# Kernel optimization log

Measured on AMD Instinct MI355X. Metric: run time of the kernel, lower is better.

## Reference

```python
import jax, jax.numpy as jnp
import numpy as np

B, T, NT, H, L, F, NH, R = 2, 1024, 30, 1024, 8, 2816, 16, 16
HD = H // NH
LORA_SCALE = 32.0 / 16.0  # lora_alpha / r
CLAMP = 10.0
EPS = 1e-6


def _rms(x, w):
    return x * jax.lax.rsqrt(jnp.mean(x * x, axis=-1, keepdims=True) + EPS) * w


def _rope(x):
    # x: [B,T,NH,HD] -- LLaMA rotary embedding
    half = HD // 2
    inv_freq = 1.0 / (10000.0 ** (jnp.arange(0, half, dtype=jnp.float32) / half))
    ang = jnp.arange(x.shape[1], dtype=jnp.float32)[:, None] * inv_freq  # [T,half]
    cos = jnp.concatenate([jnp.cos(ang), jnp.cos(ang)], -1)[None, :, None, :]
    sin = jnp.concatenate([jnp.sin(ang), jnp.sin(ang)], -1)[None, :, None, :]
    x1, x2 = x[..., :half], x[..., half:]
    return x * cos + jnp.concatenate([-x2, x1], -1) * sin


def _lora(x, W, A, Bm):
    # W: [in,out], A: [r,in], Bm: [out,r]  (dequantized base + LoRA update)
    return x @ W + ((x @ A.T) @ Bm.T) * LORA_SCALE


def setup_inputs():
    key = jax.random.key(0)
    ks = jax.random.split(key, 16)
    n = lambda k, s, sc=0.02: jax.random.normal(k, s, jnp.float32) * sc
    return {
        'x': jax.random.normal(ks[0], (B, T, NT), jnp.float32),
        'temperature': jnp.float32(1.0),
        'state_W': n(ks[1], (NT, H), 0.1),
        'state_b': jnp.zeros((H,), jnp.float32),
        'ln1': jnp.ones((L, H), jnp.float32),
        'ln2': jnp.ones((L, H), jnp.float32),
        'Wqkv': n(ks[2], (L, 3, H, H)),
        'Aqkv': n(ks[3], (L, 3, R, H)),
        'Bqkv': n(ks[4], (L, 3, H, R)),
        'Wo': n(ks[5], (L, H, H)),
        'Ao': n(ks[6], (L, R, H)),
        'Bo': n(ks[7], (L, H, R)),
        'Wgu': n(ks[8], (L, 2, H, F)),
        'Agu': n(ks[9], (L, 2, R, H)),
        'Bgu': n(ks[10], (L, 2, F, R)),
        'Wd': n(ks[11], (L, F, H)),
        'Ad': n(ks[12], (L, R, F)),
        'Bd': n(ks[13], (L, H, R)),
        'ln_f': jnp.ones((H,), jnp.float32),
        'head_W': n(ks[14], (H, NT + 1), 0.01),
        'head_b': jnp.zeros((NT + 1,), jnp.float32),
    }


def reference(x, temperature, state_W, state_b, ln1, ln2, Wqkv, Aqkv, Bqkv,
              Wo, Ao, Bo, Wgu, Agu, Bgu, Wd, Ad, Bd, ln_f, head_W, head_b):
    causal = jnp.tril(jnp.ones((T, T), bool))

    def layer(h, p):
        l1, l2, wqkv, aqkv, bqkv, wo, ao, bo, wgu, agu, bgu, wd, ad, bd = p
        hn = _rms(h, l1)
        qkv = jnp.einsum('bth,khd->kbtd', hn, wqkv)
        qkv = qkv + jnp.einsum('kbtr,kdr->kbtd',
                               jnp.einsum('bth,krh->kbtr', hn, aqkv), bqkv) * LORA_SCALE
        q = _rope(qkv[0].reshape(B, T, NH, HD))
        k = _rope(qkv[1].reshape(B, T, NH, HD))
        v = qkv[2].reshape(B, T, NH, HD)
        scores = jnp.einsum('bqhd,bkhd->bhqk', q, k) / np.sqrt(HD).astype(np.float32)
        scores = jnp.where(causal, scores, jnp.float32(-1e9))
        probs = jax.nn.softmax(scores, axis=-1)
        att = jnp.einsum('bhqk,bkhd->bqhd', probs, v).reshape(B, T, H)
        h = h + _lora(att, wo, ao, bo)
        hn2 = _rms(h, l2)
        gu = jnp.einsum('bth,khf->kbtf', hn2, wgu)
        gu = gu + jnp.einsum('kbtr,kfr->kbtf',
                             jnp.einsum('bth,krh->kbtr', hn2, agu), bgu) * LORA_SCALE
        act = jax.nn.silu(gu[0]) * gu[1]
        h = h + _lora(act, wd, ad, bd)
        return h, None

    h = x @ state_W + state_b  # state encoder -> inputs_embeds
    h, _ = jax.lax.scan(layer, h, (ln1, ln2, Wqkv, Aqkv, Bqkv, Wo, Ao, Bo,
                                   Wgu, Agu, Bgu, Wd, Ad, Bd))
    latent = _rms(h, ln_f)  # last hidden state
    logits = latent @ head_W + head_b
    logits_clamped = jnp.clip(logits, -CLAMP, CLAMP)
    portfolio_weights = jax.nn.softmax(logits_clamped / temperature, axis=-1)
    return portfolio_weights, logits_clamped
```

## Files before the change

### kernel.cpp

```cpp
#include <hip/hip_runtime.h>
#include <hip/hip_bf16.h>
#include <cstdint>

#define B_    2
#define T_    1024
#define NT_   30
#define H_    1024
#define L_    8
#define F_    2816
#define NH_   16
#define R_    16
#define HD_   64
#define M_    2048
#define NTP1_ 31

typedef unsigned short u16;
typedef short  s16x8 __attribute__((ext_vector_type(8)));
typedef unsigned short u16x4 __attribute__((ext_vector_type(4)));
typedef unsigned short u16x8 __attribute__((ext_vector_type(8)));
typedef float  f32x4 __attribute__((ext_vector_type(4)));

__device__ __forceinline__ u16 f2bf(float f){
  __hip_bfloat16 h = __float2bfloat16(f);
  return __builtin_bit_cast(unsigned short, h);
}
__device__ __forceinline__ float bf2f(u16 u){
  uint32_t v = (uint32_t)u << 16;
  return __builtin_bit_cast(float, v);
}

__device__ __forceinline__ void async16(const void* g, void* l){
  __builtin_amdgcn_global_load_lds((const __attribute__((address_space(1))) void*)g,
                                   (__attribute__((address_space(3))) void*)l, 16, 0, 0);
}

__global__ __launch_bounds__(256, 3) void fold_kernel(
    const float* __restrict__ W, const float* __restrict__ A,
    const float* __restrict__ Bm, u16* __restrict__ Wt,
    int K, int N, long strW, long strA, long strB, long strWt)
{
  const int mat = blockIdx.z;
  W  += (long)mat * strW;  A  += (long)mat * strA;
  Bm += (long)mat * strB;  Wt += (long)mat * strWt;
  const int k0 = blockIdx.x * 64, n0 = blockIdx.y * 64;
  __shared__ float Wt_s[64][65];
  __shared__ float As[16][64];
  __shared__ float Bs[64][20];
  const int tid = threadIdx.x;
  {
    const int kr = tid >> 4;
    const int n4 = (tid & 15) * 4;
    #pragma unroll
    for (int p = 0; p < 4; p++){
      int krow = p * 16 + kr;
      float4 w = *(const float4*)(W + (long)(k0 + krow) * N + n0 + n4);
      Wt_s[n4+0][krow] = w.x; Wt_s[n4+1][krow] = w.y;
      Wt_s[n4+2][krow] = w.z; Wt_s[n4+3][krow] = w.w;
    }
    const int r = tid >> 4, kc = (tid & 15) * 4;
    *(float4*)&As[r][kc] = *(const float4*)(A + (long)r * K + k0 + kc);
    const int nb = tid >> 2, r4 = (tid & 3) * 4;
    float4 b = *(const float4*)(Bm + (long)(n0 + nb) * 16 + r4);
    Bs[nb][r4+0]=b.x; Bs[nb][r4+1]=b.y; Bs[nb][r4+2]=b.z; Bs[nb][r4+3]=b.w;
  }
  __syncthreads();
  const int ko = (tid & 7) * 8;
  const int na = tid >> 3;
  float bq0[16], bq1[16];
  #pragma unroll
  for (int c = 0; c < 4; c++){
    *(float4*)&bq0[c*4] = *(const float4*)&Bs[na][c*4];
    *(float4*)&bq1[c*4] = *(const float4*)&Bs[na+32][c*4];
  }
  float l0[8] = {}, l1[8] = {};
  #pragma unroll
  for (int r = 0; r < 16; r++){
    float a[8];
    *(float4*)&a[0] = *(const float4*)&As[r][ko];
    *(float4*)&a[4] = *(const float4*)&As[r][ko+4];
    #pragma unroll
    for (int j = 0; j < 8; j++){
      l0[j] += a[j] * bq0[r];
      l1[j] += a[j] * bq1[r];
    }
  }
  u16x8 o0, o1;
  #pragma unroll
  for (int j = 0; j < 8; j++){
    o0[j] = f2bf(Wt_s[na][ko+j]    + 2.0f * l0[j]);
    o1[j] = f2bf(Wt_s[na+32][ko+j] + 2.0f * l1[j]);
  }
  *(u16x8*)(Wt + (long)(n0+na)*K    + k0 + ko) = o0;
  *(u16x8*)(Wt + (long)(n0+na+32)*K + k0 + ko) = o1;
}

__global__ __launch_bounds__(256) void embed_kernel(
    const float* __restrict__ x, const float* __restrict__ sw,
    const float* __restrict__ sb, float* __restrict__ h)
{
  const int m = blockIdx.x;
  const float* xr = x + (long)m * NT_;
  for (int jj = threadIdx.x; jj < H_; jj += 256){
    float acc = sb[jj];
    #pragma unroll
    for (int i = 0; i < NT_; i++) acc += xr[i] * sw[i * H_ + jj];
    h[(long)m * H_ + jj] = acc;
  }
}

__global__ __launch_bounds__(256) void rms_kernel(
    float* __restrict__ hsrc, const float* __restrict__ p0, const float* __restrict__ p1,
    const float* __restrict__ w, u16* __restrict__ outp, int fuse)
{
  const int m = blockIdx.x, t = threadIdx.x;
  float4 v = ((const float4*)(hsrc + (long)m * H_))[t];
  if (fuse){
    const float4 a = ((const float4*)(p0 + (long)m * H_))[t];
    const float4 b = ((const float4*)(p1 + (long)m * H_))[t];
    v.x += a.x + b.x; v.y += a.y + b.y; v.z += a.z + b.z; v.w += a.w + b.w;
    ((float4*)(hsrc + (long)m * H_))[t] = v;
  }
  float ss = v.x*v.x + v.y*v.y + v.z*v.z + v.w*v.w;
  #pragma unroll
  for (int off = 32; off >= 1; off >>= 1) ss += __shfl_xor(ss, off);
  __shared__ float red[4];
  if ((t & 63) == 0) red[t >> 6] = ss;
  __syncthreads();
  const float scale = rsqrtf((red[0]+red[1]+red[2]+red[3]) * (1.0f/H_) + 1e-6f);
  const float4 wv = ((const float4*)w)[t];
  u16x4 o;
  o[0] = f2bf(v.x*scale*wv.x); o[1] = f2bf(v.y*scale*wv.y);
  o[2] = f2bf(v.z*scale*wv.z); o[3] = f2bf(v.w*scale*wv.w);
  *(u16x4*)(outp + (long)m * H_ + t * 4) = o;
}

template<int OUTBF>
__global__ __launch_bounds__(256, 2) void gemm_bt(
    const u16* __restrict__ Ag, const u16* __restrict__ Btg, void* __restrict__ Cptr,
    int Ndim, int Klen, int Kstride, long zsA, long zsB, long zsC)
{
  Ag  += (long)blockIdx.z * zsA;
  Btg += (long)blockIdx.z * zsB;
  const int m0 = blockIdx.x * 128, n0 = blockIdx.y * 128;
  __shared__ alignas(16) u16 As[128 * 64];
  __shared__ alignas(16) u16 Bs[128 * 64];
  const int tid = threadIdx.x;
  const int wave = tid >> 6, lane = tid & 63;
  const int wm = (wave & 1) * 64, wn = (wave >> 1) * 64;
  const int fr = lane & 15, quad = lane >> 4;

  f32x4 acc[4][4] = {};

  for (int kt = 0; kt < Klen; kt += 64){
    __syncthreads();
    #pragma unroll
    for (int c = 0; c < 4; c++){
      int lin = c * 256 + tid;
      int row = lin >> 3, p = lin & 7;
      int gc = ((p ^ (row & 7)) * 8);
      async16(Ag  + (long)(m0 + row) * Kstride + kt + gc, As + lin * 8);
      async16(Btg + (long)(n0 + row) * Kstride + kt + gc, Bs + lin * 8);
    }
    __syncthreads();
    #pragma unroll
    for (int kk = 0; kk < 2; kk++){
      s16x8 af[4], bg[4];
      #pragma unroll
      for (int i = 0; i < 4; i++){
        int rA = wm + i * 16 + fr;
        af[i] = *(const s16x8*)(As + rA * 64 + (((kk*4 + quad) ^ (rA & 7)) * 8));
        int rB = wn + i * 16 + fr;
        bg[i] = *(const s16x8*)(Bs + rB * 64 + (((kk*4 + quad) ^ (rB & 7)) * 8));
      }
      #pragma unroll
      for (int i = 0; i < 4; i++)
        #pragma unroll
        for (int j = 0; j < 4; j++)
          acc[i][j] = __builtin_amdgcn_mfma_f32_16x16x32_bf16(af[i], bg[j], acc[i][j], 0, 0, 0);
    }
  }
  #pragma unroll
  for (int i = 0; i < 4; i++){
    int row0 = m0 + wm + i * 16 + quad * 4;
    #pragma unroll
    for (int j = 0; j < 4; j++){
      int col = n0 + wn + j * 16 + fr;
      #pragma unroll
      for (int r = 0; r < 4; r++){
        long idx = (long)(row0 + r) * Ndim + col;
        if (OUTBF){
          u16* C = (u16*)Cptr + (long)blockIdx.z * zsC;
          C[idx] = f2bf(acc[i][j][r]);
        } else {
          float* C = (float*)Cptr + (long)blockIdx.z * zsC;
          C[idx] = acc[i][j][r];
        }
      }
    }
  }
}

__global__ __launch_bounds__(256, 2) void gemm_gu(
    const u16* __restrict__ Ag, const u16* __restrict__ Bgw,
    const u16* __restrict__ Buw, u16* __restrict__ actb)
{
  const int m0 = blockIdx.x * 128, n0 = blockIdx.y * 128;
  __shared__ alignas(16) u16 As[128 * 64];
  __shared__ alignas(16) u16 Bg_[128 * 64];
  __shared__ alignas(16) u16 Bu_[128 * 64];
  const int tid = threadIdx.x;
  const int wave = tid >> 6, lane = tid & 63;
  const int wm = (wave & 1) * 64, wn = (wave >> 1) * 64;
  const int fr = lane & 15, quad = lane >> 4;

  f32x4 accg[4][4] = {}, accu[4][4] = {};

  for (int kt = 0; kt < H_; kt += 64){
    __syncthreads();
    #pragma unroll
    for (int c = 0; c < 4; c++){
      int lin = c * 256 + tid;
      int row = lin >> 3, p = lin & 7;
      int gc = ((p ^ (row & 7)) * 8);
      async16(Ag  + (long)(m0 + row) * H_ + kt + gc, As  + lin * 8);
      async16(Bgw + (long)(n0 + row) * H_ + kt + gc, Bg_ + lin * 8);
      async16(Buw + (long)(n0 + row) * H_ + kt + gc, Bu_ + lin * 8);
    }
    __syncthreads();
    #pragma unroll
    for (int kk = 0; kk < 2; kk++){
      s16x8 af[4], bb[4];
      #pragma unroll
      for (int i = 0; i < 4; i++){
        int rA = wm + i * 16 + fr;
        af[i] = *(const s16x8*)(As + rA * 64 + (((kk*4 + quad) ^ (rA & 7)) * 8));
      }
      #pragma unroll
      for (int i = 0; i < 4; i++){
        int rB = wn + i * 16 + fr;
        bb[i] = *(const s16x8*)(Bg_ + rB * 64 + (((kk*4 + quad) ^ (rB & 7)) * 8));
      }
      #pragma unroll
      for (int i = 0; i < 4; i++)
        #pragma unroll
        for (int j = 0; j < 4; j++)
          accg[i][j] = __builtin_amdgcn_mfma_f32_16x16x32_bf16(af[i], bb[j], accg[i][j], 0, 0, 0);
      #pragma unroll
      for (int i = 0; i < 4; i++){
        int rB = wn + i * 16 + fr;
        bb[i] = *(const s16x8*)(Bu_ + rB * 64 + (((kk*4 + quad) ^ (rB & 7)) * 8));
      }
      #pragma unroll
      for (int i = 0; i < 4; i++)
        #pragma unroll
        for (int j = 0; j < 4; j++)
          accu[i][j] = __builtin_amdgcn_mfma_f32_16x16x32_bf16(af[i], bb[j], accu[i][j], 0, 0, 0);
    }
  }
  #pragma unroll
  for (int i = 0; i < 4; i++){
    int row0 = m0 + wm + i * 16 + quad * 4;
    #pragma unroll
    for (int j = 0; j < 4; j++){
      int col = n0 + wn + j * 16 + fr;
      #pragma unroll
      for (int r = 0; r < 4; r++){
        float g = accg[i][j][r], u = accu[i][j][r];
        float act = g / (1.0f + __expf(-g)) * u;
        actb[(long)(row0 + r) * F_ + col] = f2bf(act);
      }
    }
  }
}

__global__ __launch_bounds__(256) void rope_kernel(
    const u16* __restrict__ qkv, u16* __restrict__ qr, u16* __restrict__ kr)
{
  const int m = blockIdx.x;
  const int b = m >> 10, t = m & 1023;
  for (int w = threadIdx.x; w < 1024; w += 256){
    const int sel = w >> 9;
    const int hh  = (w >> 5) & 15;
    const int i   = w & 31;
    const u16* src = qkv + (long)sel * M_ * H_ + (long)m * H_ + hh * HD_;
    float x1 = bf2f(src[i]), x2 = bf2f(src[i + 32]);
    float freq = exp2f((float)i * (-13.287712379549449f / 32.0f));
    float ang = (float)t * freq;
    float sn, cs; __sincosf(ang, &sn, &cs);
    u16* dst = (sel ? kr : qr) + ((long)((b * NH_ + hh) * T_ + t)) * HD_;
    dst[i]      = f2bf(x1 * cs - x2 * sn);
    dst[i + 32] = f2bf(x2 * cs + x1 * sn);
  }
}

__global__ __launch_bounds__(256) void vtrans_kernel(
    const u16* __restrict__ qkv, u16* __restrict__ vt)
{
  const int bh = blockIdx.x, b = bh >> 4, hh = bh & 15;
  const int d = threadIdx.x & 63, tc = threadIdx.x >> 6;
  const int t0 = blockIdx.y * 32 + tc * 8;
  const u16* src = qkv + (long)2 * M_ * H_ + (long)b * T_ * H_ + hh * HD_ + d;
  u16x8 o;
  #pragma unroll
  for (int j = 0; j < 8; j++) o[j] = src[(long)(t0 + j) * H_];
  *(u16x8*)(vt + ((long)bh * HD_ + d) * T_ + t0) = o;
}

__global__ __launch_bounds__(256, 2) void attn_kernel(
    const u16* __restrict__ qr, const u16* __restrict__ kr,
    const u16* __restrict__ vt, u16* __restrict__ att)
{
  const int qt = blockIdx.x;
  const int bh = blockIdx.y;
  const int b = bh >> 4, hh = bh & 15;
  __shared__ alignas(16) u16 Qs[64 * 64];
  __shared__ alignas(16) u16 Ks[128 * 64];
  __shared__ alignas(16) u16 Vs[64 * 128];
  __shared__ alignas(16) u16 Ps[64 * 136];
  const int tid = threadIdx.x;
  const int wave = tid >> 6, lane = tid & 63, fr = lane & 15, quad = lane >> 4;
  const int wrow = wave * 16;

  const u16* qg = qr + ((long)bh * T_ + qt * 64) * HD_;
  #pragma unroll
  for (int c = 0; c < 2; c++){
    int lin = c * 256 + tid, row = lin >> 3, p = lin & 7;
    async16(qg + row * HD_ + ((p ^ (row & 7)) * 8), Qs + lin * 8);
  }
  f32x4 o_acc[4] = {};
  float m_r[4] = {-1e30f, -1e30f, -1e30f, -1e30f};
  float l_r[4] = {};
  const u16* kgb = kr + (long)bh * T_ * HD_;
  const u16* vgb = vt + (long)bh * HD_ * T_;
  const int kmax = (qt * 64 + 63) >> 7;

  for (int kt = 0; kt <= kmax; kt++){
    __syncthreads();
    const u16* kg = kgb + (long)kt * 128 * HD_;
    #pragma unroll
    for (int c = 0; c < 4; c++){
      int lin = c * 256 + tid, row = lin >> 3, p = lin & 7;
      async16(kg + row * HD_ + ((p ^ (row & 7)) * 8), Ks + lin * 8);
    }
    #pragma unroll
    for (int c = 0; c < 4; c++){
      int lin = c * 256 + tid, row = lin >> 4, p = lin & 15;
      async16(vgb + (long)row * T_ + kt * 128 + ((p ^ (row & 15)) * 8), Vs + lin * 8);
    }
    __syncthreads();

    f32x4 s[8] = {};
    s16x8 aq[2];
    {
      int rA = wrow + fr;
      #pragma unroll
      for (int kk = 0; kk < 2; kk++)
        aq[kk] = *(const s16x8*)(Qs + rA * 64 + (((kk*4 + quad) ^ (rA & 7)) * 8));
    }
    #pragma unroll
    for (int ik = 0; ik < 8; ik++){
      #pragma unroll
      for (int kk = 0; kk < 2; kk++){
        int rB = ik * 16 + fr;
        s16x8 bk = *(const s16x8*)(Ks + rB * 64 + (((kk*4 + quad) ^ (rB & 7)) * 8));
        s[ik] = __builtin_amdgcn_mfma_f32_16x16x32_bf16(aq[kk], bk, s[ik], 0, 0, 0);
      }
    }
    const bool diag = (kt == kmax);
    #pragma unroll
    for (int r = 0; r < 4; r++){
      const int qgi = qt * 64 + wrow + quad * 4 + r;
      float tmax = -1e30f;
      #pragma unroll
      for (int ik = 0; ik < 8; ik++){
        float v = s[ik][r] * 0.125f;
        if (diag && (kt * 128 + ik * 16 + fr) > qgi) v = -1e9f;
        s[ik][r] = v;
        tmax = fmaxf(tmax, v);
      }
      #pragma unroll
      for (int off = 8; off >= 1; off >>= 1) tmax = fmaxf(tmax, __shfl_xor(tmax, off));
      const float mnew = fmaxf(m_r[r], tmax);
      const float alpha = __expf(m_r[r] - mnew);
      m_r[r] = mnew;
      float ts = 0.0f;
      const int prow = wrow + quad * 4 + r;
      #pragma unroll
      for (int ik = 0; ik < 8; ik++){
        float p = __expf(s[ik][r] - mnew);
        ts += p;
        Ps[prow * 136 + ik * 16 + fr] = f2bf(p);
      }
      #pragma unroll
      for (int off = 8; off >= 1; off >>= 1) ts += __shfl_xor(ts, off);
      l_r[r] = l_r[r] * alpha + ts;
      #pragma unroll
      for (int jd = 0; jd < 4; jd++) o_acc[jd][r] *= alpha;
    }
    #pragma unroll
    for (int kk2 = 0; kk2 < 4; kk2++){
      s16x8 ap = *(const s16x8*)(Ps + (wrow + fr) * 136 + kk2 * 32 + quad * 8);
      #pragma unroll
      for (int jd = 0; jd < 4; jd++){
        int rV = jd * 16 + fr;
        s16x8 bv = *(const s16x8*)(Vs + rV * 128 + (((kk2*4 + quad) ^ (rV & 15)) * 8));
        o_acc[jd] = __builtin_amdgcn_mfma_f32_16x16x32_bf16(ap, bv, o_acc[jd], 0, 0, 0);
      }
    }
  }
  #pragma unroll
  for (int r = 0; r < 4; r++){
    const int t_loc = qt * 64 + wrow + quad * 4 + r;
    const long rowbase = ((long)b * T_ + t_loc) * H_ + hh * HD_;
    const float inv = 1.0f / l_r[r];
    #pragma unroll
    for (int jd = 0; jd < 4; jd++)
      att[rowbase + jd * 16 + fr] = f2bf(o_acc[jd][r] * inv);
  }
}

__global__ __launch_bounds__(256) void head_kernel(
    const float* __restrict__ hsrc, const float* __restrict__ p0, const float* __restrict__ p1,
    const float* __restrict__ lnf, const float* __restrict__ hw, const float* __restrict__ hb,
    const float* __restrict__ temp, float* __restrict__ outp)
{
  const int m = blockIdx.x, t = threadIdx.x;
  __shared__ float lat[H_];
  __shared__ float red[4];
  __shared__ float part[8][32];
  float4 v = ((const float4*)(hsrc + (long)m * H_))[t];
  {
    const float4 a = ((const float4*)(p0 + (long)m * H_))[t];
    const float4 b = ((const float4*)(p1 + (long)m * H_))[t];
    v.x += a.x + b.x; v.y += a.y + b.y; v.z += a.z + b.z; v.w += a.w + b.w;
  }
  float ss = v.x*v.x + v.y*v.y + v.z*v.z + v.w*v.w;
  #pragma unroll
  for (int off = 32; off >= 1; off >>= 1) ss += __shfl_xor(ss, off);
  if ((t & 63) == 0) red[t >> 6] = ss;
  __syncthreads();
  const float scale = rsqrtf((red[0]+red[1]+red[2]+red[3]) * (1.0f/H_) + 1e-6f);
  const float4 wv = ((const float4*)lnf)[t];
  lat[t*4+0] = v.x*scale*wv.x;  lat[t*4+1] = v.y*scale*wv.y;
  lat[t*4+2] = v.z*scale*wv.z;  lat[t*4+3] = v.w*scale*wv.w;
  __syncthreads();
  const int j = t & 31, seg = t >> 5;
  float p = 0.0f;
  if (j < 31){
    const float* wp = hw + j;
    for (int k = seg * 128; k < seg * 128 + 128; k++) p += lat[k] * wp[(long)k * 31];
  }
  part[seg][j] = p;
  __syncthreads();
  if (t < 32){
    float dot = 0.0f;
    #pragma unroll
    for (int s2 = 0; s2 < 8; s2++) dot += part[s2][t];
    const float logit = (t < 31) ? dot + hb[t] : -1e30f;
    const float lc = fminf(fmaxf(logit, -10.0f), 10.0f);
    const float z = (t < 31) ? lc / temp[0] : -1e30f;
    float mx = z;
    #pragma unroll
    for (int off = 16; off >= 1; off >>= 1) mx = fmaxf(mx, __shfl_xor(mx, off, 32));
    const float e = (t < 31) ? __expf(z - mx) : 0.0f;
    float sum = e;
    #pragma unroll
    for (int off = 16; off >= 1; off >>= 1) sum += __shfl_xor(sum, off, 32);
    if (t < 31){
      outp[(long)m * NTP1_ + t] = e / sum;
      outp[(long)M_ * NTP1_ + (long)m * NTP1_ + t] = lc;
    }
  }
}

extern "C" void kernel_launch(void* const* d_in, const int* in_sizes, int n_in,
                              void* d_out, int out_size, void* d_ws, size_t ws_size,
                              hipStream_t stream) {
  const float* x    = (const float*)d_in[0];
  const float* temp = (const float*)d_in[1];
  const float* sW   = (const float*)d_in[2];
  const float* sb   = (const float*)d_in[3];
  const float* ln1  = (const float*)d_in[4];
  const float* ln2  = (const float*)d_in[5];
  const float* Wqkv = (const float*)d_in[6];
  const float* Aqkv = (const float*)d_in[7];
  const float* Bqkv = (const float*)d_in[8];
  const float* Wo   = (const float*)d_in[9];
  const float* Ao   = (const float*)d_in[10];
  const float* Bo   = (const float*)d_in[11];
  const float* Wgu  = (const float*)d_in[12];
  const float* Agu  = (const float*)d_in[13];
  const float* Bgu  = (const float*)d_in[14];
  const float* Wd   = (const float*)d_in[15];
  const float* Ad   = (const float*)d_in[16];
  const float* Bd   = (const float*)d_in[17];
  const float* lnf  = (const float*)d_in[18];
  const float* hW   = (const float*)d_in[19];
  const float* hb   = (const float*)d_in[20];
  float* out = (float*)d_out;

  uint8_t* ws = (uint8_t*)d_ws;
  size_t off = 0;
  auto alloc = [&](size_t bytes) -> void* {
    void* p = ws + off;
    off += (bytes + 255) & ~(size_t)255;
    return p;
  };
  u16*   wt_qkv = (u16*)  alloc((size_t)L_ * 3 * H_ * H_ * 2);
  u16*   wt_o   = (u16*)  alloc((size_t)L_ * H_ * H_ * 2);
  u16*   wt_gu  = (u16*)  alloc((size_t)L_ * 2 * F_ * H_ * 2);
  u16*   wt_d   = (u16*)  alloc((size_t)L_ * H_ * F_ * 2);
  float* h      = (float*)alloc((size_t)M_ * H_ * 4);
  u16*   hn     = (u16*)  alloc((size_t)M_ * H_ * 2);
  u16*   qkvb   = (u16*)  alloc((size_t)3 * M_ * H_ * 2);
  float* p0     = (float*)alloc((size_t)2 * M_ * H_ * 4);
  float* p1     = p0 + (size_t)M_ * H_;
  u16*   qr     = (u16*)  alloc((size_t)M_ * H_ * 2);
  u16*   krr    = (u16*)  alloc((size_t)M_ * H_ * 2);
  u16*   vtb    = (u16*)  alloc((size_t)M_ * H_ * 2);
  u16*   attb   = (u16*)  alloc((size_t)M_ * H_ * 2);
  u16*   actb   = (u16*)  alloc((size_t)M_ * F_ * 2);

  fold_kernel<<<dim3(16, 16, L_ * 3), 256, 0, stream>>>(Wqkv, Aqkv, Bqkv, wt_qkv,
      H_, H_, (long)H_ * H_, (long)R_ * H_, (long)H_ * R_, (long)H_ * H_);
  fold_kernel<<<dim3(16, 16, L_), 256, 0, stream>>>(Wo, Ao, Bo, wt_o,
      H_, H_, (long)H_ * H_, (long)R_ * H_, (long)H_ * R_, (long)H_ * H_);
  fold_kernel<<<dim3(16, 44, L_ * 2), 256, 0, stream>>>(Wgu, Agu, Bgu, wt_gu,
      H_, F_, (long)H_ * F_, (long)R_ * H_, (long)F_ * R_, (long)F_ * H_);
  fold_kernel<<<dim3(44, 16, L_), 256, 0, stream>>>(Wd, Ad, Bd, wt_d,
      F_, H_, (long)F_ * H_, (long)R_ * F_, (long)H_ * R_, (long)H_ * F_);

  embed_kernel<<<M_, 256, 0, stream>>>(x, sW, sb, h);

  for (int l = 0; l < L_; l++){
    rms_kernel<<<M_, 256, 0, stream>>>(h, p0, p1, ln1 + (long)l * H_, hn, l > 0 ? 1 : 0);
    gemm_bt<1><<<dim3(16, 8, 3), 256, 0, stream>>>(hn, wt_qkv + (long)l * 3 * H_ * H_,
        qkvb, H_, H_, H_, 0, (long)H_ * H_, (long)M_ * H_);
    rope_kernel<<<M_, 256, 0, stream>>>(qkvb, qr, krr);
    vtrans_kernel<<<dim3(B_ * NH_, T_ / 32), 256, 0, stream>>>(qkvb, vtb);
    attn_kernel<<<dim3(T_ / 64, B_ * NH_), 256, 0, stream>>>(qr, krr, vtb, attb);
    gemm_bt<0><<<dim3(16, 8, 2), 256, 0, stream>>>(attb, wt_o + (long)l * H_ * H_,
        p0, H_, 512, H_, 512, 512, (long)M_ * H_);
    rms_kernel<<<M_, 256, 0, stream>>>(h, p0, p1, ln2 + (long)l * H_, hn, 1);
    gemm_gu<<<dim3(16, 22), 256, 0, stream>>>(hn,
        wt_gu + (long)l * 2 * F_ * H_, wt_gu + (long)l * 2 * F_ * H_ + (long)F_ * H_, actb);
    gemm_bt<0><<<dim3(16, 8, 2), 256, 0, stream>>>(actb, wt_d + (long)l * H_ * F_,
        p0, H_, 1408, F_, 1408, 1408, (long)M_ * H_);
  }

  head_kernel<<<M_, 256, 0, stream>>>(h, p0, p1, lnf, hW, hb, temp, out);
}
```

Measured before the change: 1.728 ms.

## Split-K QKV GEMM, fuse rope with V transpose, pair causal attention tiles

The QKV projection becomes a split-K GEMM with fp32 partials, launched as a 16x24x2 grid instead of 16x8x3, so it has more blocks. A new fused kernel sums the two partials and does both the rotary embedding and the V transpose in one launch. Each attention block now handles query tile i and tile 15-i, which balances the causal work and halves the grid. The cost is fp32 partial traffic of about 50MB per layer and a lower attention block count, which may leave CUs idle.

```diff
diff --git a/kernel.cpp b/kernel.cpp
--- a/kernel.cpp
+++ b/kernel.cpp
@@ -273,44 +273,49 @@
   }
 }
 
-__global__ __launch_bounds__(256) void rope_kernel(
-    const u16* __restrict__ qkv, u16* __restrict__ qr, u16* __restrict__ kr)
-{
-  const int m = blockIdx.x;
-  const int b = m >> 10, t = m & 1023;
-  for (int w = threadIdx.x; w < 1024; w += 256){
-    const int sel = w >> 9;
-    const int hh  = (w >> 5) & 15;
-    const int i   = w & 31;
-    const u16* src = qkv + (long)sel * M_ * H_ + (long)m * H_ + hh * HD_;
-    float x1 = bf2f(src[i]), x2 = bf2f(src[i + 32]);
-    float freq = exp2f((float)i * (-13.287712379549449f / 32.0f));
-    float ang = (float)t * freq;
-    float sn, cs; __sincosf(ang, &sn, &cs);
-    u16* dst = (sel ? kr : qr) + ((long)((b * NH_ + hh) * T_ + t)) * HD_;
-    dst[i]      = f2bf(x1 * cs - x2 * sn);
-    dst[i + 32] = f2bf(x2 * cs + x1 * sn);
-  }
-}
-
-__global__ __launch_bounds__(256) void vtrans_kernel(
-    const u16* __restrict__ qkv, u16* __restrict__ vt)
-{
-  const int bh = blockIdx.x, b = bh >> 4, hh = bh & 15;
-  const int d = threadIdx.x & 63, tc = threadIdx.x >> 6;
-  const int t0 = blockIdx.y * 32 + tc * 8;
-  const u16* src = qkv + (long)2 * M_ * H_ + (long)b * T_ * H_ + hh * HD_ + d;
-  u16x8 o;
-  #pragma unroll
-  for (int j = 0; j < 8; j++) o[j] = src[(long)(t0 + j) * H_];
-  *(u16x8*)(vt + ((long)bh * HD_ + d) * T_ + t0) = o;
+__global__ __launch_bounds__(256) void rope_vt_kernel(
+    const float* __restrict__ pq, u16* __restrict__ qr, u16* __restrict__ kr,
+    u16* __restrict__ vt)
+{
+  const int bid = blockIdx.x;
+  if (bid < M_){
+    const int m = bid;
+    const int b = m >> 10, t = m & 1023;
+    for (int w = threadIdx.x; w < 1024; w += 256){
+      const int sel = w >> 9;
+      const int hh  = (w >> 5) & 15;
+      const int i   = w & 31;
+      const float* s0 = pq + (long)m * 3072 + sel * 1024 + hh * HD_;
+      const float* s1 = s0 + (long)M_ * 3072;
+      float x1 = s0[i] + s1[i];
+      float x2 = s0[i + 32] + s1[i + 32];
+      float freq = exp2f((float)i * (-13.287712379549449f / 32.0f));
+      float ang = (float)t * freq;
+      float sn, cs; __sincosf(ang, &sn, &cs);
+      u16* dst = (sel ? kr : qr) + ((long)((b * NH_ + hh) * T_ + t)) * HD_;
+      dst[i]      = f2bf(x1 * cs - x2 * sn);
+      dst[i + 32] = f2bf(x2 * cs + x1 * sn);
+    }
+  } else {
+    const int v = bid - M_;
+    const int bh = v >> 5, tch = v & 31;
+    const int b = bh >> 4, hh = bh & 15;
+    const int d = threadIdx.x & 63, tc = threadIdx.x >> 6;
+    const int t0 = tch * 32 + tc * 8;
+    u16x8 o;
+    #pragma unroll
+    for (int j = 0; j < 8; j++){
+      long idx = (long)(b * T_ + t0 + j) * 3072 + 2048 + hh * HD_ + d;
+      o[j] = f2bf(pq[idx] + pq[idx + (long)M_ * 3072]);
+    }
+    *(u16x8*)(vt + ((long)bh * HD_ + d) * T_ + t0) = o;
+  }
 }
 
 __global__ __launch_bounds__(256, 2) void attn_kernel(
     const u16* __restrict__ qr, const u16* __restrict__ kr,
     const u16* __restrict__ vt, u16* __restrict__ att)
 {
-  const int qt = blockIdx.x;
   const int bh = blockIdx.y;
   const int b = bh >> 4, hh = bh & 15;
   __shared__ alignas(16) u16 Qs[64 * 64];
@@ -320,102 +325,106 @@
   const int tid = threadIdx.x;
   const int wave = tid >> 6, lane = tid & 63, fr = lane & 15, quad = lane >> 4;
   const int wrow = wave * 16;
-
-  const u16* qg = qr + ((long)bh * T_ + qt * 64) * HD_;
-  #pragma unroll
-  for (int c = 0; c < 2; c++){
-    int lin = c * 256 + tid, row = lin >> 3, p = lin & 7;
-    async16(qg + row * HD_ + ((p ^ (row & 7)) * 8), Qs + lin * 8);
-  }
-  f32x4 o_acc[4] = {};
-  float m_r[4] = {-1e30f, -1e30f, -1e30f, -1e30f};
-  float l_r[4] = {};
   const u16* kgb = kr + (long)bh * T_ * HD_;
   const u16* vgb = vt + (long)bh * HD_ * T_;
-  const int kmax = (qt * 64 + 63) >> 7;
-
-  for (int kt = 0; kt <= kmax; kt++){
+
+  for (int pass = 0; pass < 2; pass++){
+    const int qt = pass ? (15 - (int)blockIdx.x) : (int)blockIdx.x;
     __syncthreads();
-    const u16* kg = kgb + (long)kt * 128 * HD_;
-    #pragma unroll
-    for (int c = 0; c < 4; c++){
+    const u16* qg = qr + ((long)bh * T_ + qt * 64) * HD_;
+    #pragma unroll
+    for (int c = 0; c < 2; c++){
       int lin = c * 256 + tid, row = lin >> 3, p = lin & 7;
-      async16(kg + row * HD_ + ((p ^ (row & 7)) * 8), Ks + lin * 8);
-    }
-    #pragma unroll
-    for (int c = 0; c < 4; c++){
-      int lin = c * 256 + tid, row = lin >> 4, p = lin & 15;
-      async16(vgb + (long)row * T_ + kt * 128 + ((p ^ (row & 15)) * 8), Vs + lin * 8);
-    }
-    __syncthreads();
-
-    f32x4 s[8] = {};
-    s16x8 aq[2];
-    {
-      int rA = wrow + fr;
-      #pragma unroll
-      for (int kk = 0; kk < 2; kk++)
-        aq[kk] = *(const s16x8*)(Qs + rA * 64 + (((kk*4 + quad) ^ (rA & 7)) * 8));
-    }
-    #pragma unroll
-    for (int ik = 0; ik < 8; ik++){
-      #pragma unroll
-      for (int kk = 0; kk < 2; kk++){
-        int rB = ik * 16 + fr;
-        s16x8 bk = *(const s16x8*)(Ks + rB * 64 + (((kk*4 + quad) ^ (rB & 7)) * 8));
-        s[ik] = __builtin_amdgcn_mfma_f32_16x16x32_bf16(aq[kk], bk, s[ik], 0, 0, 0);
-      }
-    }
-    const bool diag = (kt == kmax);
+      async16(qg + row * HD_ + ((p ^ (row & 7)) * 8), Qs + lin * 8);
+    }
+    f32x4 o_acc[4] = {};
+    float m_r[4] = {-1e30f, -1e30f, -1e30f, -1e30f};
+    float l_r[4] = {};
+    const int kmax = (qt * 64 + 63) >> 7;
+
+    for (int kt = 0; kt <= kmax; kt++){
+      __syncthreads();
+      const u16* kg = kgb + (long)kt * 128 * HD_;
+      #pragma unroll
+      for (int c = 0; c < 4; c++){
+        int lin = c * 256 + tid, row = lin >> 3, p = lin & 7;
+        async16(kg + row * HD_ + ((p ^ (row & 7)) * 8), Ks + lin * 8);
+      }
+      #pragma unroll
+      for (int c = 0; c < 4; c++){
+        int lin = c * 256 + tid, row = lin >> 4, p = lin & 15;
+        async16(vgb + (long)row * T_ + kt * 128 + ((p ^ (row & 15)) * 8), Vs + lin * 8);
+      }
+      __syncthreads();
+
+      f32x4 s[8] = {};
+      s16x8 aq[2];
+      {
+        int rA = wrow + fr;
+        #pragma unroll
+        for (int kk = 0; kk < 2; kk++)
+          aq[kk] = *(const s16x8*)(Qs + rA * 64 + (((kk*4 + quad) ^ (rA & 7)) * 8));
+      }
+      #pragma unroll
+      for (int ik = 0; ik < 8; ik++){
+        #pragma unroll
+        for (int kk = 0; kk < 2; kk++){
+          int rB = ik * 16 + fr;
+          s16x8 bk = *(const s16x8*)(Ks + rB * 64 + (((kk*4 + quad) ^ (rB & 7)) * 8));
+          s[ik] = __builtin_amdgcn_mfma_f32_16x16x32_bf16(aq[kk], bk, s[ik], 0, 0, 0);
+        }
+      }
+      const bool diag = (kt == kmax);
+      #pragma unroll
+      for (int r = 0; r < 4; r++){
+        const int qgi = qt * 64 + wrow + quad * 4 + r;
+        float tmax = -1e30f;
+        #pragma unroll
+        for (int ik = 0; ik < 8; ik++){
+          float v = s[ik][r] * 0.125f;
+          if (diag && (kt * 128 + ik * 16 + fr) > qgi) v = -1e9f;
+          s[ik][r] = v;
+          tmax = fmaxf(tmax, v);
+        }
+        #pragma unroll
+        for (int off = 8; off >= 1; off >>= 1) tmax = fmaxf(tmax, __shfl_xor(tmax, off));
+        const float mnew = fmaxf(m_r[r], tmax);
+        const float alpha = __expf(m_r[r] - mnew);
+        m_r[r] = mnew;
+        float ts = 0.0f;
+        const int prow = wrow + quad * 4 + r;
+        #pragma unroll
+        for (int ik = 0; ik < 8; ik++){
+          float p = __expf(s[ik][r] - mnew);
+          ts += p;
+          Ps[prow * 136 + ik * 16 + fr] = f2bf(p);
+        }
+        #pragma unroll
+        for (int off = 8; off >= 1; off >>= 1) ts += __shfl_xor(ts, off);
+        l_r[r] = l_r[r] * alpha + ts;
+        #pragma unroll
+        for (int jd = 0; jd < 4; jd++) o_acc[jd][r] *= alpha;
+      }
+      #pragma unroll
+      for (int kk2 = 0; kk2 < 4; kk2++){
+        s16x8 ap = *(const s16x8*)(Ps + (wrow + fr) * 136 + kk2 * 32 + quad * 8);
+        #pragma unroll
+        for (int jd = 0; jd < 4; jd++){
+          int rV = jd * 16 + fr;
+          s16x8 bv = *(const s16x8*)(Vs + rV * 128 + (((kk2*4 + quad) ^ (rV & 15)) * 8));
+          o_acc[jd] = __builtin_amdgcn_mfma_f32_16x16x32_bf16(ap, bv, o_acc[jd], 0, 0, 0);
+        }
+      }
+    }
     #pragma unroll
     for (int r = 0; r < 4; r++){
-      const int qgi = qt * 64 + wrow + quad * 4 + r;
-      float tmax = -1e30f;
-      #pragma unroll
-      for (int ik = 0; ik < 8; ik++){
-        float v = s[ik][r] * 0.125f;
-        if (diag && (kt * 128 + ik * 16 + fr) > qgi) v = -1e9f;
-        s[ik][r] = v;
-        tmax = fmaxf(tmax, v);
-      }
-      #pragma unroll
-      for (int off = 8; off >= 1; off >>= 1) tmax = fmaxf(tmax, __shfl_xor(tmax, off));
-      const float mnew = fmaxf(m_r[r], tmax);
-      const float alpha = __expf(m_r[r] - mnew);
-      m_r[r] = mnew;
-      float ts = 0.0f;
-      const int prow = wrow + quad * 4 + r;
-      #pragma unroll
-      for (int ik = 0; ik < 8; ik++){
-        float p = __expf(s[ik][r] - mnew);
-        ts += p;
-        Ps[prow * 136 + ik * 16 + fr] = f2bf(p);
-      }
-      #pragma unroll
-      for (int off = 8; off >= 1; off >>= 1) ts += __shfl_xor(ts, off);
-      l_r[r] = l_r[r] * alpha + ts;
-      #pragma unroll
-      for (int jd = 0; jd < 4; jd++) o_acc[jd][r] *= alpha;
-    }
-    #pragma unroll
-    for (int kk2 = 0; kk2 < 4; kk2++){
-      s16x8 ap = *(const s16x8*)(Ps + (wrow + fr) * 136 + kk2 * 32 + quad * 8);
-      #pragma unroll
-      for (int jd = 0; jd < 4; jd++){
-        int rV = jd * 16 + fr;
-        s16x8 bv = *(const s16x8*)(Vs + rV * 128 + (((kk2*4 + quad) ^ (rV & 15)) * 8));
-        o_acc[jd] = __builtin_amdgcn_mfma_f32_16x16x32_bf16(ap, bv, o_acc[jd], 0, 0, 0);
-      }
-    }
-  }
-  #pragma unroll
-  for (int r = 0; r < 4; r++){
-    const int t_loc = qt * 64 + wrow + quad * 4 + r;
-    const long rowbase = ((long)b * T_ + t_loc) * H_ + hh * HD_;
-    const float inv = 1.0f / l_r[r];
-    #pragma unroll
-    for (int jd = 0; jd < 4; jd++)
-      att[rowbase + jd * 16 + fr] = f2bf(o_acc[jd][r] * inv);
+      const int t_loc = qt * 64 + wrow + quad * 4 + r;
+      const long rowbase = ((long)b * T_ + t_loc) * H_ + hh * HD_;
+      const float inv = 1.0f / l_r[r];
+      #pragma unroll
+      for (int jd = 0; jd < 4; jd++)
+        att[rowbase + jd * 16 + fr] = f2bf(o_acc[jd][r] * inv);
+    }
   }
 }
 
@@ -445,12 +454,12 @@
   lat[t*4+2] = v.z*scale*wv.z;  lat[t*4+3] = v.w*scale*wv.w;
   __syncthreads();
   const int j = t & 31, seg = t >> 5;
-  float p = 0.0f;
+  float pp = 0.0f;
   if (j < 31){
     const float* wp = hw + j;
-    for (int k = seg * 128; k < seg * 128 + 128; k++) p += lat[k] * wp[(long)k * 31];
-  }
-  part[seg][j] = p;
+    for (int k = seg * 128; k < seg * 128 + 128; k++) pp += lat[k] * wp[(long)k * 31];
+  }
+  part[seg][j] = pp;
   __syncthreads();
   if (t < 32){
     float dot = 0.0f;
@@ -512,7 +521,7 @@
   u16*   wt_d   = (u16*)  alloc((size_t)L_ * H_ * F_ * 2);
   float* h      = (float*)alloc((size_t)M_ * H_ * 4);
   u16*   hn     = (u16*)  alloc((size_t)M_ * H_ * 2);
-  u16*   qkvb   = (u16*)  alloc((size_t)3 * M_ * H_ * 2);
+  float* pq     = (float*)alloc((size_t)2 * M_ * 3072 * 4);
   float* p0     = (float*)alloc((size_t)2 * M_ * H_ * 4);
   float* p1     = p0 + (size_t)M_ * H_;
   u16*   qr     = (u16*)  alloc((size_t)M_ * H_ * 2);
@@ -534,11 +543,10 @@
 
   for (int l = 0; l < L_; l++){
     rms_kernel<<<M_, 256, 0, stream>>>(h, p0, p1, ln1 + (long)l * H_, hn, l > 0 ? 1 : 0);
-    gemm_bt<1><<<dim3(16, 8, 3), 256, 0, stream>>>(hn, wt_qkv + (long)l * 3 * H_ * H_,
-        qkvb, H_, H_, H_, 0, (long)H_ * H_, (long)M_ * H_);
-    rope_kernel<<<M_, 256, 0, stream>>>(qkvb, qr, krr);
-    vtrans_kernel<<<dim3(B_ * NH_, T_ / 32), 256, 0, stream>>>(qkvb, vtb);
-    attn_kernel<<<dim3(T_ / 64, B_ * NH_), 256, 0, stream>>>(qr, krr, vtb, attb);
+    gemm_bt<0><<<dim3(16, 24, 2), 256, 0, stream>>>(hn, wt_qkv + (long)l * 3 * H_ * H_,
+        pq, 3072, 512, H_, 512, 512, (long)M_ * 3072);
+    rope_vt_kernel<<<M_ + 1024, 256, 0, stream>>>(pq, qr, krr, vtb);
+    attn_kernel<<<dim3(8, B_ * NH_), 256, 0, stream>>>(qr, krr, vtb, attb);
     gemm_bt<0><<<dim3(16, 8, 2), 256, 0, stream>>>(attb, wt_o + (long)l * H_ * H_,
         p0, H_, 512, H_, 512, 512, (long)M_ * H_);
     rms_kernel<<<M_, 256, 0, stream>>>(h, p0, p1, ln2 + (long)l * H_, hn, 1);
```

After: 1.741 ms. About the same (+0.8%).
